# Kernel tuning notes

Measured on AMD Instinct MI355X. Metric: run time of the kernel, lower is better.

Reference implementation:

```python
import jax, jax.numpy as jnp
from jax import lax
import numpy as np

LSTM = 128      # encoder hidden per direction
H2 = 2 * LSTM   # decoder hidden / bi-encoder output dim
E = 1024        # embedding dim
V = 30611       # vocab
A = 64          # attention dim
B, S, T = 16, 400, 96
START_TOK = 101


def setup_inputs() -> dict:
    key = jax.random.key(0)
    ks = jax.random.split(key, 24)
    d = {}
    d["word_embedding"] = jax.random.normal(ks[0], (V, E), jnp.float32) * 0.05
    d["article"] = jax.random.randint(ks[1], (B, S), 0, V)
    d["article_length"] = jax.random.randint(ks[2], (B,), S // 2, S + 1)
    d["abstract"] = jax.random.randint(ks[3], (B, T), 0, V)

    def p(k, shape, scale):
        return jax.random.normal(k, shape, jnp.float32) * scale

    # encoder BiLSTM (PyTorch gate order i,f,g,o), forward and backward dirs
    d["enc_Wih_f"] = p(ks[4], (4 * LSTM, E), 0.03)
    d["enc_Whh_f"] = p(ks[5], (4 * LSTM, LSTM), 0.08)
    d["enc_b_f"] = jnp.zeros((4 * LSTM,), jnp.float32)
    d["enc_Wih_b"] = p(ks[6], (4 * LSTM, E), 0.03)
    d["enc_Whh_b"] = p(ks[7], (4 * LSTM, LSTM), 0.08)
    d["enc_b_b"] = jnp.zeros((4 * LSTM,), jnp.float32)
    # decoder LSTM: input = embed(1024) + context(256)
    d["dec_Wih"] = p(ks[8], (4 * H2, E + H2), 0.03)
    d["dec_Whh"] = p(ks[9], (4 * H2, H2), 0.06)
    d["dec_b"] = jnp.zeros((4 * H2,), jnp.float32)
    # vocab prediction
    d["pred_W"] = p(ks[10], (V, H2), 0.06)
    d["pred_b"] = jnp.zeros((V,), jnp.float32)
    # additive attention
    d["attn_s_W"] = p(ks[11], (A, H2), 0.06)
    d["attn_s_b"] = jnp.zeros((A,), jnp.float32)
    d["attn_h_W"] = p(ks[12], (A, H2), 0.06)
    d["attn_h_b"] = jnp.zeros((A,), jnp.float32)
    d["attn_f_W"] = p(ks[13], (1, A), 0.12)
    d["attn_f_b"] = jnp.zeros((1,), jnp.float32)
    return d


def _lstm_cell(x, h, c, Wih, Whh, b):
    g = x @ Wih.T + h @ Whh.T + b
    i, f, gg, o = jnp.split(g, 4, axis=-1)
    c = jax.nn.sigmoid(f) * c + jax.nn.sigmoid(i) * jnp.tanh(gg)
    h = jax.nn.sigmoid(o) * jnp.tanh(c)
    return h, c


def reference(word_embedding, article, article_length, abstract,
              enc_Wih_f, enc_Whh_f, enc_b_f, enc_Wih_b, enc_Whh_b, enc_b_b,
              dec_Wih, dec_Whh, dec_b, pred_W, pred_b,
              attn_s_W, attn_s_b, attn_h_W, attn_h_b, attn_f_W, attn_f_b):
    dt = word_embedding.dtype
    # ---- encoder ----
    xe = word_embedding[article]          # [B,S,E]
    xs = xe.transpose(1, 0, 2)            # [S,B,E]
    z = jnp.zeros((B, LSTM), dt)

    def fstep(carry, x):
        h, c = carry
        h, c = _lstm_cell(x, h, c, enc_Wih_f, enc_Whh_f, enc_b_f)
        return (h, c), h

    def bstep(carry, x):
        h, c = carry
        h, c = _lstm_cell(x, h, c, enc_Wih_b, enc_Whh_b, enc_b_b)
        return (h, c), h

    (hf, cf_f), out_f = lax.scan(fstep, (z, z), xs)
    (hb, cf_b), out_b = lax.scan(bstep, (z, z), xs, reverse=True)
    enc_out = jnp.concatenate([out_f, out_b], axis=-1).transpose(1, 0, 2)  # [B,S,2H]

    # decoder init state = concat of final fwd/bwd encoder states
    h0 = jnp.concatenate([hf, hb], axis=-1)   # [B,H2]
    c0 = jnp.concatenate([cf_f, cf_b], axis=-1)

    # attention mask: (+9999 valid, -9999 pad); min(score, mask) keeps valid scores
    length = jnp.clip(article_length, 1, S)
    pos = jnp.arange(S)
    mask = jnp.where(pos[None, :] < length[:, None], 9999.0, -9999.0).astype(dt)

    enc_ws = enc_out @ attn_s_W.T + attn_s_b  # [B,S,A], precomputed per original code

    # teacher forcing inputs: step 0 uses token 101, step t uses abstract[:, t-1]
    tokens_in = jnp.concatenate(
        [jnp.full((B, 1), START_TOK, dtype=abstract.dtype), abstract[:, :-1]], axis=1)
    emb_in = word_embedding[tokens_in].transpose(1, 0, 2)  # [T,B,E]

    def dstep(carry, emb):
        h, c, ctx = carry
        x = jnp.concatenate([emb, ctx], axis=-1)           # [B,E+H2]
        h, c = _lstm_cell(x, h, c, dec_Wih, dec_Whh, dec_b)
        logits = h @ pred_W.T + pred_b                     # [B,V]
        wh = h @ attn_h_W.T + attn_h_b                     # [B,A]
        score = jnp.tanh(enc_ws + wh[:, None, :]) @ attn_f_W[0] + attn_f_b[0]  # [B,S]
        score = jnp.minimum(score, mask)
        w = jax.nn.softmax(score, axis=-1)
        ctx = jnp.einsum('bs,bsd->bd', w, enc_out)         # [B,H2]
        return (h, c, ctx), logits

    ctx0 = jnp.zeros((B, H2), dt)
    _, logits = lax.scan(dstep, (h0, c0, ctx0), emb_in)    # [T,B,V]

    logits = logits.transpose(1, 0, 2).reshape(B * T, V)
    tgt = abstract.reshape(-1)
    logp = jax.nn.log_softmax(logits, axis=-1)
    nll = -jnp.take_along_axis(logp, tgt[:, None], axis=1)[:, 0]
    valid = (tgt != 0).astype(logits.dtype)                # ignore_index=0
    loss = jnp.sum(nll * valid) / jnp.maximum(jnp.sum(valid), 1.0)
    return loss
```

## Files before the change

kernel.cpp:

```cpp
#include <hip/hip_runtime.h>
#include <cmath>

#define NB 16
#define SS 400
#define TT 96
#define HL 128
#define HH 256
#define AA 64
#define VV 30611
#define VVP 30720
#define START_TOK 101
#define NCHUNK 120

typedef __attribute__((ext_vector_type(8))) short bf16x8;
typedef __attribute__((ext_vector_type(4))) float f32x4;

#define PIN4(v) asm volatile("" : "+v"((v).x), "+v"((v).y), "+v"((v).z), "+v"((v).w))
#define LBAR() asm volatile("s_waitcnt lgkmcnt(0)\n\ts_barrier" ::: "memory")

__device__ __forceinline__ float gload(const float* p) {
  return __hip_atomic_load(p, __ATOMIC_RELAXED, __HIP_MEMORY_SCOPE_AGENT);
}
__device__ __forceinline__ void gstore(float* p, float v) {
  __hip_atomic_store(p, v, __ATOMIC_RELAXED, __HIP_MEMORY_SCOPE_AGENT);
}
__device__ __forceinline__ float sigmf(float x) { return 1.0f / (1.0f + __expf(-x)); }
__device__ __forceinline__ float tanhf_(float x) {
  float xc = fminf(fmaxf(x, -15.0f), 15.0f);
  return 1.0f - 2.0f / (__expf(2.0f * xc) + 1.0f);
}
__device__ __forceinline__ short f2bf(float f) {
  unsigned u = __float_as_uint(f);
  unsigned r = (u + 0x7FFFu + ((u >> 16) & 1u)) >> 16;
  return (short)r;
}
__device__ __forceinline__ void flagbar(int* flags, int b, int g, int target) {
  __syncthreads();
  if (threadIdx.x == 0)
    __hip_atomic_store(&flags[b*8 + g], target, __ATOMIC_RELAXED, __HIP_MEMORY_SCOPE_AGENT);
  if (threadIdx.x < 8) {
    while (__hip_atomic_load(&flags[b*8 + threadIdx.x], __ATOMIC_RELAXED, __HIP_MEMORY_SCOPE_AGENT) < target)
      __builtin_amdgcn_s_sleep(1);
  }
  LBAR();
}

__global__ __launch_bounds__(256) void k_init(int* flags) {
  if (threadIdx.x < 128) flags[threadIdx.x] = 0;
}

__global__ __launch_bounds__(256) void k_casts(
    const float* __restrict__ wf, const float* __restrict__ wb,
    const float* __restrict__ dwih,
    short* __restrict__ wfB, short* __restrict__ wbB, short* __restrict__ dwB)
{
  const int stride = gridDim.x * 256;
  const int t0 = blockIdx.x * 256 + threadIdx.x;
  for (int i = t0; i < 512*1024; i += stride) wfB[i] = f2bf(wf[i]);
  for (int i = t0; i < 512*1024; i += stride) wbB[i] = f2bf(wb[i]);
  for (int i = t0; i < 1024*1024; i += stride) {
    int r = i >> 10, k = i & 1023;
    dwB[i] = f2bf(dwih[r*1280 + k]);
  }
}

__global__ __launch_bounds__(256) void k_embproj_enc_mfma(
    const float* __restrict__ emb, const int* __restrict__ article,
    const short* __restrict__ wfB, const short* __restrict__ wbB,
    const float* __restrict__ bf, const float* __restrict__ bb,
    float* __restrict__ xcomb)
{
  const int m0 = blockIdx.x * 64;
  const int n0 = blockIdx.y * 256;
  const int t = threadIdx.x;
  const int w = t >> 6, l = t & 63;
  __shared__ short Abuf[64*136];
  __shared__ int tok[64];
  if (t < 64) {
    int R = m0 + t, s = R >> 4, b = R & 15;
    tok[t] = article[b*SS + s];
  }
  const short* __restrict__ Wb = (n0 < 512) ? wfB : wbB;
  const int nb0 = (n0 < 512) ? n0 : (n0 - 512);
  f32x4 acc[4][4];
  #pragma unroll
  for (int i = 0; i < 4; ++i)
    #pragma unroll
    for (int j = 0; j < 4; ++j) acc[i][j] = (f32x4){0.f,0.f,0.f,0.f};
  __syncthreads();
  const int ar = t >> 2, ak0 = (t & 3) * 32;
  for (int kc = 0; kc < 8; ++kc) {
    const float* src = emb + (size_t)tok[ar]*1024 + kc*128 + ak0;
    #pragma unroll
    for (int j = 0; j < 8; ++j) {
      float4 v = *(const float4*)(src + 4*j);
      short4 s4; s4.x = f2bf(v.x); s4.y = f2bf(v.y); s4.z = f2bf(v.z); s4.w = f2bf(v.w);
      *(short4*)(&Abuf[ar*136 + ak0 + 4*j]) = s4;
    }
    LBAR();
    #pragma unroll
    for (int ks = 0; ks < 4; ++ks) {
      bf16x8 af[4];
      #pragma unroll
      for (int mr = 0; mr < 4; ++mr)
        af[mr] = *(const bf16x8*)(&Abuf[(mr*16 + (l & 15))*136 + ks*32 + (l >> 4)*8]);
      #pragma unroll
      for (int ct = 0; ct < 4; ++ct) {
        int n = nb0 + w*64 + ct*16 + (l & 15);
        bf16x8 bfr = *(const bf16x8*)(Wb + (size_t)n*1024 + kc*128 + ks*32 + (l >> 4)*8);
        #pragma unroll
        for (int mr = 0; mr < 4; ++mr)
          acc[mr][ct] = __builtin_amdgcn_mfma_f32_16x16x32_bf16(af[mr], bfr, acc[mr][ct], 0, 0, 0);
      }
    }
    LBAR();
  }
  #pragma unroll
  for (int ct = 0; ct < 4; ++ct) {
    int n = n0 + w*64 + ct*16 + (l & 15);
    float bias = (n < 512) ? bf[n] : bb[n - 512];
    #pragma unroll
    for (int mr = 0; mr < 4; ++mr) {
      #pragma unroll
      for (int r = 0; r < 4; ++r) {
        int R = m0 + mr*16 + (l >> 4)*4 + r;
        xcomb[(size_t)R*1024 + n] = acc[mr][ct][r] + bias;
      }
    }
  }
}

__global__ __launch_bounds__(256) void k_embproj_dec_mfma(
    const float* __restrict__ emb, const int* __restrict__ abstr,
    const short* __restrict__ dwB, const float* __restrict__ db,
    float* __restrict__ decpre)
{
  const int m0 = blockIdx.x * 64;
  const int n0 = blockIdx.y * 256;
  const int t = threadIdx.x;
  const int w = t >> 6, l = t & 63;
  __shared__ short Abuf[64*136];
  __shared__ int tok[64];
  if (t < 64) {
    int R = m0 + t, tt = R >> 4, b = R & 15;
    tok[t] = (tt == 0) ? START_TOK : abstr[b*TT + tt - 1];
  }
  f32x4 acc[4][4];
  #pragma unroll
  for (int i = 0; i < 4; ++i)
    #pragma unroll
    for (int j = 0; j < 4; ++j) acc[i][j] = (f32x4){0.f,0.f,0.f,0.f};
  __syncthreads();
  const int ar = t >> 2, ak0 = (t & 3) * 32;
  for (int kc = 0; kc < 8; ++kc) {
    const float* src = emb + (size_t)tok[ar]*1024 + kc*128 + ak0;
    #pragma unroll
    for (int j = 0; j < 8; ++j) {
      float4 v = *(const float4*)(src + 4*j);
      short4 s4; s4.x = f2bf(v.x); s4.y = f2bf(v.y); s4.z = f2bf(v.z); s4.w = f2bf(v.w);
      *(short4*)(&Abuf[ar*136 + ak0 + 4*j]) = s4;
    }
    LBAR();
    #pragma unroll
    for (int ks = 0; ks < 4; ++ks) {
      bf16x8 af[4];
      #pragma unroll
      for (int mr = 0; mr < 4; ++mr)
        af[mr] = *(const bf16x8*)(&Abuf[(mr*16 + (l & 15))*136 + ks*32 + (l >> 4)*8]);
      #pragma unroll
      for (int ct = 0; ct < 4; ++ct) {
        int n = n0 + w*64 + ct*16 + (l & 15);
        bf16x8 bfr = *(const bf16x8*)(dwB + (size_t)n*1024 + kc*128 + ks*32 + (l >> 4)*8);
        #pragma unroll
        for (int mr = 0; mr < 4; ++mr)
          acc[mr][ct] = __builtin_amdgcn_mfma_f32_16x16x32_bf16(af[mr], bfr, acc[mr][ct], 0, 0, 0);
      }
    }
    LBAR();
  }
  #pragma unroll
  for (int ct = 0; ct < 4; ++ct) {
    int n = n0 + w*64 + ct*16 + (l & 15);
    float bias = db[n];
    #pragma unroll
    for (int mr = 0; mr < 4; ++mr) {
      #pragma unroll
      for (int r = 0; r < 4; ++r) {
        int R = m0 + mr*16 + (l >> 4)*4 + r;
        decpre[(size_t)R*1024 + n] = acc[mr][ct][r] + bias;
      }
    }
  }
}

__global__ __launch_bounds__(1024, 4) void k_encoder(
    const float* __restrict__ xcomb,
    const float* __restrict__ whhf, const float* __restrict__ whhb,
    float* __restrict__ encout,
    float* __restrict__ hpub,
    float* __restrict__ c0buf,
    const float* __restrict__ predW, short* __restrict__ predWb)
{
  const int t = threadIdx.x;
  if (blockIdx.x >= 32) {
    const size_t idx0 = (size_t)(blockIdx.x - 32) * 1024 + t;
    const size_t stride = (size_t)224 * 1024;
    for (size_t i = idx0; i < (size_t)VVP*256; i += stride)
      predWb[i] = (i < (size_t)VV*256) ? f2bf(predW[i]) : (short)0;
    return;
  }
  const int b = blockIdx.x & 15, dir = blockIdx.x >> 4;
  const int row = t & 511;
  const int ks = t >> 9;
  const float* __restrict__ Whh = dir ? whhb : whhf;
  float4 wr[16];
  #pragma unroll
  for (int j = 0; j < 16; ++j) {
    wr[j] = *(const float4*)(Whh + row*128 + ks*64 + j*4);
    PIN4(wr[j]);
  }
  __shared__ float hl[128];
  __shared__ float part[2][512];
  float c_reg = 0.0f;
  if (t < 128) hl[t] = 0.0f;
  float xv0 = 0.f, xv1 = 0.f, xv2 = 0.f, xv3 = 0.f;
  if (t < 128) {
    const float* xr = xcomb + ((dir ? (SS-1) : 0)*NB + b)*1024 + dir*512 + t;
    xv0 = xr[0]; xv1 = xr[128]; xv2 = xr[256]; xv3 = xr[384];
  }
  __syncthreads();
  for (int s = 0; s < SS; ++s) {
    const int sf = dir ? (SS-1-s) : s;
    const float* hs = hl + ks*64;
    float a0 = 0.f, a1 = 0.f, a2 = 0.f, a3 = 0.f;
    #pragma unroll
    for (int j = 0; j < 16; j += 4) {
      float4 h0 = *(const float4*)(hs + j*4);
      float4 h1 = *(const float4*)(hs + j*4 + 4);
      float4 h2 = *(const float4*)(hs + j*4 + 8);
      float4 h3 = *(const float4*)(hs + j*4 + 12);
      a0 += wr[j].x*h0.x + wr[j].y*h0.y + wr[j].z*h0.z + wr[j].w*h0.w;
      a1 += wr[j+1].x*h1.x + wr[j+1].y*h1.y + wr[j+1].z*h1.z + wr[j+1].w*h1.w;
      a2 += wr[j+2].x*h2.x + wr[j+2].y*h2.y + wr[j+2].z*h2.z + wr[j+2].w*h2.w;
      a3 += wr[j+3].x*h3.x + wr[j+3].y*h3.y + wr[j+3].z*h3.z + wr[j+3].w*h3.w;
    }
    part[ks][row] = (a0 + a1) + (a2 + a3);
    float nx0 = 0.f, nx1 = 0.f, nx2 = 0.f, nx3 = 0.f;
    if (t < 128 && s + 1 < SS) {
      const int sfn = dir ? (SS-2-s) : (s+1);
      const float* xr = xcomb + (sfn*NB + b)*1024 + dir*512 + t;
      nx0 = xr[0]; nx1 = xr[128]; nx2 = xr[256]; nx3 = xr[384];
    }
    LBAR();
    if (t < 128) {
      float gi = part[0][t]       + part[1][t]       + xv0;
      float gf = part[0][128 + t] + part[1][128 + t] + xv1;
      float gg = part[0][256 + t] + part[1][256 + t] + xv2;
      float go = part[0][384 + t] + part[1][384 + t] + xv3;
      float iv = sigmf(gi), fv = sigmf(gf), gv = tanhf_(gg), ov = sigmf(go);
      c_reg = fv*c_reg + iv*gv;
      float hv = ov*tanhf_(c_reg);
      hl[t] = hv;
      encout[(b*SS + sf)*HH + dir*HL + t] = hv;
    }
    LBAR();
    xv0 = nx0; xv1 = nx1; xv2 = nx2; xv3 = nx3;
  }
  if (t < 128) {
    hpub[b*HH + dir*HL + t] = hl[t];
    c0buf[b*HH + dir*HL + t] = c_reg;
  }
}

__global__ __launch_bounds__(256) void k_encws(
    const float* __restrict__ encout,
    const float* __restrict__ asW, const float* __restrict__ asb,
    float* __restrict__ encwsR)
{
  const int rt = blockIdx.x;
  const int tid = threadIdx.x;
  __shared__ float Al[32*260];
  #pragma unroll
  for (int i = 0; i < 32; ++i) {
    int l = tid + i*256;
    int r = l >> 8, k = l & 255;
    Al[r*260 + k] = encout[(rt*32 + r)*256 + k];
  }
  __syncthreads();
  const int a = tid & 63, rg = tid >> 6;
  float acc[8];
  #pragma unroll
  for (int q = 0; q < 8; ++q) acc[q] = 0.0f;
  const float4* w4 = (const float4*)(asW + a*256);
  for (int k4 = 0; k4 < 64; ++k4) {
    float4 w = w4[k4];
    #pragma unroll
    for (int q = 0; q < 8; ++q) {
      const float4* a4 = (const float4*)(Al + (rg*8 + q)*260);
      float4 av = a4[k4];
      acc[q] += av.x*w.x + av.y*w.y + av.z*w.z + av.w*w.w;
    }
  }
  float bias = asb[a];
  #pragma unroll
  for (int q = 0; q < 8; ++q) {
    int row = rt*32 + rg*8 + q;
    encwsR[row*64 + a] = acc[q] + bias;
  }
}

__global__ __launch_bounds__(1024, 4) void k_decoder(
    const float* __restrict__ decpre,
    const float* __restrict__ dwhh,
    const float* __restrict__ dwih,
    const float* __restrict__ ahW, const float* __restrict__ ahb,
    const float* __restrict__ afW, const float* __restrict__ afb,
    const float* __restrict__ encwsR,
    const float* __restrict__ encout,
    const int* __restrict__ alen,
    const float* __restrict__ c0buf,
    float* hpub, float* cpub, float* wpub,
    float* __restrict__ dhall,
    int* flags)
{
  const int wg = blockIdx.x;
  const int g = wg >> 4, b = wg & 15;
  const int t = threadIdx.x;
  const int r = t & 127, ks = t >> 7;
  const int lane = t & 63;
  const int u = t & 31;
  const int s0 = g*50;

  const int grow = (r >> 5)*256 + g*32 + (r & 31);
  float4 wr[16];
  #pragma unroll
  for (int j = 0; j < 16; ++j) {
    int k = ks*64 + j*4;
    wr[j] = (k < 256) ? *(const float4*)(dwhh + grow*256 + k)
                      : *(const float4*)(dwih + grow*1280 + 1024 + (k - 256));
    PIN4(wr[j]);
  }

  __shared__ float encl[50*256];
  __shared__ float wsl[50*68];
  __shared__ float ahWt[32*68];
  __shared__ float hc[512];
  __shared__ float part[8][132];
  __shared__ float wh[64];
  __shared__ float fwl[64];
  __shared__ float scl[64];
  __shared__ float sh_m, sh_s;

  for (int i = t; i < 50*256; i += 1024) {
    int si = i >> 8, d = i & 255;
    encl[i] = encout[(b*SS + s0 + si)*HH + d];
  }
  for (int i = t; i < 50*64; i += 1024) {
    int si = i >> 6, a = i & 63;
    wsl[si*68 + a] = encwsR[(b*SS + s0 + si)*64 + a];
  }
  for (int i = t; i < 32*64; i += 1024) {
    int u2 = i >> 6, a = i & 63;
    ahWt[u2*68 + a] = ahW[a*HH + g*32 + u2];
  }
  if (t < 64) fwl[t] = afW[t];
  const float fb0 = afb[0];
  int len = alen[b]; len = min(max(len, 1), SS);
  float c_reg = 0.f;
  float pre0 = 0.f, pre1 = 0.f, pre2 = 0.f, pre3 = 0.f;
  if (t < 256) {
    c_reg = c0buf[b*HH + g*32 + u];
    hc[t] = gload(hpub + b*HH + t);
    hc[256 + t] = 0.0f;
    const float* pr = decpre + (size_t)(0*NB + b)*1024 + g*32 + u;
    pre0 = pr[0]; pre1 = pr[256]; pre2 = pr[512]; pre3 = pr[768];
  }
  __syncthreads();

  for (int tt = 0; tt < TT; ++tt) {
    {
      const float* hs = hc + ks*64;
      float a0 = 0.f, a1 = 0.f, a2 = 0.f, a3 = 0.f;
      #pragma unroll
      for (int j = 0; j < 16; j += 4) {
        float4 h0 = *(const float4*)(hs + j*4);
        float4 h1 = *(const float4*)(hs + j*4 + 4);
        float4 h2 = *(const float4*)(hs + j*4 + 8);
        float4 h3 = *(const float4*)(hs + j*4 + 12);
        a0 += wr[j].x*h0.x + wr[j].y*h0.y + wr[j].z*h0.z + wr[j].w*h0.w;
        a1 += wr[j+1].x*h1.x + wr[j+1].y*h1.y + wr[j+1].z*h1.z + wr[j+1].w*h1.w;
        a2 += wr[j+2].x*h2.x + wr[j+2].y*h2.y + wr[j+2].z*h2.z + wr[j+2].w*h2.w;
        a3 += wr[j+3].x*h3.x + wr[j+3].y*h3.y + wr[j+3].z*h3.z + wr[j+3].w*h3.w;
      }
      part[ks][r] = (a0 + a1) + (a2 + a3);
    }
    LBAR();
    if (t < 256) {
      float g0 = pre0, g1 = pre1, g2 = pre2, g3 = pre3;
      #pragma unroll
      for (int j = 0; j < 8; ++j) {
        g0 += part[j][u];
        g1 += part[j][32 + u];
        g2 += part[j][64 + u];
        g3 += part[j][96 + u];
      }
      float iv = sigmf(g0), fv = sigmf(g1), gv = tanhf_(g2), ov = sigmf(g3);
      c_reg = fv*c_reg + iv*gv;
      float hv = ov*tanhf_(c_reg);
      if (t < 32) {
        gstore(hpub + b*HH + g*32 + t, hv);
        dhall[(tt*NB + b)*HH + g*32 + t] = hv;
      }
      int wv = t >> 6;
      int a = wv*16 + (lane >> 2);
      int j4 = lane & 3;
      float wacc = 0.f;
      #pragma unroll
      for (int i = 0; i < 8; ++i) {
        int u2 = j4*8 + i;
        float hx = __shfl(hv, u2, 64);
        wacc += ahWt[u2*68 + a] * hx;
      }
      wacc += __shfl_xor(wacc, 1);
      wacc += __shfl_xor(wacc, 2);
      if (j4 == 0) gstore(wpub + (b*8 + g)*72 + a, wacc);
    }
    flagbar(flags, b, g, 2*tt + 1);
    if (t < 256) {
      hc[t] = gload(hpub + b*HH + t);
      if (tt + 1 < TT) {
        const float* pr = decpre + (size_t)((tt+1)*NB + b)*1024 + g*32 + u;
        pre0 = pr[0]; pre1 = pr[256]; pre2 = pr[512]; pre3 = pr[768];
      }
    } else if (t < 320) {
      int a = t - 256;
      float s = ahb[a];
      #pragma unroll
      for (int j = 0; j < 8; ++j) s += gload(wpub + (b*8 + j)*72 + a);
      wh[a] = s;
    }
    LBAR();
    if (t < 800) {
      int s = t >> 4, j = t & 15;
      const float* wrow = wsl + s*68 + j*4;
      float p = fwl[j*4]   * tanhf_(wrow[0] + wh[j*4])
              + fwl[j*4+1] * tanhf_(wrow[1] + wh[j*4+1])
              + fwl[j*4+2] * tanhf_(wrow[2] + wh[j*4+2])
              + fwl[j*4+3] * tanhf_(wrow[3] + wh[j*4+3]);
      p += __shfl_xor(p, 1);
      p += __shfl_xor(p, 2);
      p += __shfl_xor(p, 4);
      p += __shfl_xor(p, 8);
      if (j == 0) scl[s] = p;
    }
    LBAR();
    if (t < 64) {
      float sc = -1e30f;
      if (t < 50) {
        sc = fb0 + scl[t];
        sc = fminf(sc, (s0 + t < len) ? 9999.0f : -9999.0f);
      }
      float m = sc;
      #pragma unroll
      for (int o = 32; o; o >>= 1) m = fmaxf(m, __shfl_xor(m, o));
      float p = (t < 50) ? __expf(sc - m) : 0.0f;
      scl[t] = p;
      float ssum = p;
      #pragma unroll
      for (int o = 32; o; o >>= 1) ssum += __shfl_xor(ssum, o);
      if (t == 0) { sh_m = m; sh_s = ssum; }
    }
    LBAR();
    if (t < 256) {
      float acc = 0.0f;
      const float* eb = encl + t;
      #pragma unroll 10
      for (int i = 0; i < 50; ++i) acc += scl[i] * eb[i*256];
      gstore(cpub + (b*8 + g)*272 + t, acc);
      if (t == 0) gstore(cpub + (b*8 + g)*272 + 256, sh_m);
      if (t == 1) gstore(cpub + (b*8 + g)*272 + 257, sh_s);
    }
    flagbar(flags, b, g, 2*tt + 2);
    if (t < 256) {
      float mj[8], sj[8];
      #pragma unroll
      for (int j = 0; j < 8; ++j) {
        mj[j] = gload(cpub + (b*8 + j)*272 + 256);
        sj[j] = gload(cpub + (b*8 + j)*272 + 257);
      }
      float M = mj[0];
      #pragma unroll
      for (int j = 1; j < 8; ++j) M = fmaxf(M, mj[j]);
      float denom = 0.f, ctx = 0.f;
      #pragma unroll
      for (int j = 0; j < 8; ++j) {
        float e = __expf(mj[j] - M);
        denom += sj[j] * e;
        ctx += gload(cpub + (b*8 + j)*272 + t) * e;
      }
      hc[256 + t] = ctx / denom;
    }
    LBAR();
  }
}

__global__ __launch_bounds__(256) void k_pred_mfma(
    const float* __restrict__ dhall,
    const short* __restrict__ predWb,
    const float* __restrict__ predb,
    float* __restrict__ pm, float* __restrict__ ps)
{
  const int m0 = blockIdx.x * 64;
  const int ch = blockIdx.y;
  const int c0 = ch * 256;
  const int t = threadIdx.x;
  const int w = t >> 6, l = t & 63;
  __shared__ __align__(16) char smem[64*264*4];
  short* Abuf = (short*)smem;
  float* L    = (float*)smem;
  __shared__ float red[256];
  __shared__ float rowmax[64];

  {
    const int ar = t >> 2, ak0 = (t & 3) * 64;
    const float* src = dhall + (size_t)(m0 + ar)*256 + ak0;
    #pragma unroll
    for (int j = 0; j < 16; ++j) {
      float4 v = *(const float4*)(src + 4*j);
      short4 s4; s4.x = f2bf(v.x); s4.y = f2bf(v.y); s4.z = f2bf(v.z); s4.w = f2bf(v.w);
      *(short4*)(&Abuf[ar*264 + ak0 + 4*j]) = s4;
    }
  }
  LBAR();
  f32x4 acc[4][4];
  #pragma unroll
  for (int i = 0; i < 4; ++i)
    #pragma unroll
    for (int j = 0; j < 4; ++j) acc[i][j] = (f32x4){0.f,0.f,0.f,0.f};
  #pragma unroll
  for (int kst = 0; kst < 8; ++kst) {
    bf16x8 af[4];
    #pragma unroll
    for (int mr = 0; mr < 4; ++mr)
      af[mr] = *(const bf16x8*)(&Abuf[(mr*16 + (l & 15))*264 + kst*32 + (l >> 4)*8]);
    #pragma unroll
    for (int ct = 0; ct < 4; ++ct) {
      int col = c0 + w*64 + ct*16 + (l & 15);
      bf16x8 bfr = *(const bf16x8*)(predWb + (size_t)col*256 + kst*32 + (l >> 4)*8);
      #pragma unroll
      for (int mr = 0; mr < 4; ++mr)
        acc[mr][ct] = __builtin_amdgcn_mfma_f32_16x16x32_bf16(af[mr], bfr, acc[mr][ct], 0, 0, 0);
    }
  }
  LBAR();
  #pragma unroll
  for (int ct = 0; ct < 4; ++ct) {
    int col = c0 + w*64 + ct*16 + (l & 15);
    float bias = (col < VV) ? predb[col] : 0.0f;
    bool valid = (col < VV);
    #pragma unroll
    for (int mr = 0; mr < 4; ++mr) {
      #pragma unroll
      for (int r = 0; r < 4; ++r) {
        int rl = mr*16 + (l >> 4)*4 + r;
        L[rl*264 + w*64 + ct*16 + (l & 15)] = valid ? (acc[mr][ct][r] + bias) : -1e30f;
      }
    }
  }
  LBAR();
  {
    const int row = t & 63, qd = t >> 6;
    float m = -1e30f;
    const float* Lr = L + row*264 + qd*64;
    for (int i = 0; i < 64; ++i) m = fmaxf(m, Lr[i]);
    red[qd*64 + row] = m;
  }
  LBAR();
  if (t < 64) {
    float m = fmaxf(fmaxf(red[t], red[64+t]), fmaxf(red[128+t], red[192+t]));
    rowmax[t] = m;
  }
  LBAR();
  {
    const int row = t & 63, qd = t >> 6;
    float m = rowmax[row];
    float ssum = 0.f;
    const float* Lr = L + row*264 + qd*64;
    for (int i = 0; i < 64; ++i) ssum += __expf(Lr[i] - m);
    red[qd*64 + row] = ssum;
  }
  LBAR();
  if (t < 64) {
    float ssum = red[t] + red[64+t] + red[128+t] + red[192+t];
    pm[(m0 + t)*NCHUNK + ch] = rowmax[t];
    ps[(m0 + t)*NCHUNK + ch] = ssum;
  }
}

__global__ __launch_bounds__(256) void k_loss_part(
    const float* __restrict__ pm, const float* __restrict__ ps,
    const float* __restrict__ dhall,
    const float* __restrict__ predW, const float* __restrict__ predb,
    const int* __restrict__ abstr, float* __restrict__ lpart)
{
  const int tid = threadIdx.x;
  const int row = blockIdx.x*256 + tid;
  __shared__ float rs[256], rc[256];
  float lsum = 0.0f, lcnt = 0.0f;
  {
    int t = row >> 4, b = row & 15;
    int tok = abstr[b*TT + t];
    float m = -1e30f;
    for (int c = 0; c < NCHUNK; ++c) m = fmaxf(m, pm[row*NCHUNK + c]);
    float ss = 0.0f;
    for (int c = 0; c < NCHUNK; ++c) ss += ps[row*NCHUNK + c] * __expf(pm[row*NCHUNK + c] - m);
    float lse = m + __logf(ss);
    float tl = predb[tok];
    const float* hrow = dhall + row*256;
    const float* wrow = predW + tok*256;
    #pragma unroll 4
    for (int k = 0; k < 256; ++k) tl += hrow[k] * wrow[k];
    if (tok != 0) { lsum = lse - tl; lcnt = 1.0f; }
  }
  rs[tid] = lsum; rc[tid] = lcnt;
  __syncthreads();
  for (int st = 128; st; st >>= 1) {
    if (tid < st) { rs[tid] += rs[tid + st]; rc[tid] += rc[tid + st]; }
    __syncthreads();
  }
  if (tid == 0) { lpart[blockIdx.x*2] = rs[0]; lpart[blockIdx.x*2 + 1] = rc[0]; }
}

__global__ void k_loss_final(const float* __restrict__ lpart, float* __restrict__ out) {
  if (threadIdx.x == 0) {
    float s = 0.f, c = 0.f;
    for (int i = 0; i < 6; ++i) { s += lpart[i*2]; c += lpart[i*2 + 1]; }
    out[0] = s / fmaxf(c, 1.0f);
  }
}

extern "C" void kernel_launch(void* const* d_in, const int* in_sizes, int n_in,
                              void* d_out, int out_size, void* d_ws, size_t ws_size,
                              hipStream_t stream) {
  const float* emb   = (const float*)d_in[0];
  const int* article = (const int*)d_in[1];
  const int* alen    = (const int*)d_in[2];
  const int* abstr   = (const int*)d_in[3];
  const float* eWihF = (const float*)d_in[4];
  const float* eWhhF = (const float*)d_in[5];
  const float* ebF   = (const float*)d_in[6];
  const float* eWihB = (const float*)d_in[7];
  const float* eWhhB = (const float*)d_in[8];
  const float* ebB   = (const float*)d_in[9];
  const float* dWih  = (const float*)d_in[10];
  const float* dWhh  = (const float*)d_in[11];
  const float* db    = (const float*)d_in[12];
  const float* pW    = (const float*)d_in[13];
  const float* pb    = (const float*)d_in[14];
  const float* asW   = (const float*)d_in[15];
  const float* asb   = (const float*)d_in[16];
  const float* ahW   = (const float*)d_in[17];
  const float* ahb   = (const float*)d_in[18];
  const float* afW   = (const float*)d_in[19];
  const float* afb   = (const float*)d_in[20];
  float* out = (float*)d_out;

  float* w = (float*)d_ws;
  size_t o = 0;
  float* xcomb  = w + o; o += (size_t)SS*NB*1024;
  float* encout = w + o; o += (size_t)NB*SS*HH;
  float* encwsR = w + o; o += (size_t)NB*SS*AA;
  float* decpre = w + o; o += (size_t)TT*NB*1024;
  float* dhall  = w + o; o += (size_t)TT*NB*HH;
  float* hpub   = w + o; o += NB*HH;
  float* cpub   = w + o; o += NB*8*272;
  float* wpub   = w + o; o += NB*8*72;
  float* c0buf  = w + o; o += NB*HH;
  float* pm     = w + o; o += (size_t)TT*NB*NCHUNK;
  float* ps     = w + o; o += (size_t)TT*NB*NCHUNK;
  float* lpart  = w + o; o += 16;
  int* flags = (int*)(w + o); o += 128;
  short* predWb = (short*)(w + o); o += (size_t)VVP*256/2;
  short* wfB    = (short*)(w + o); o += 512*1024/2;
  short* wbB    = (short*)(w + o); o += 512*1024/2;
  short* dwB    = (short*)(w + o); o += 1024*1024/2;

  k_init<<<1, 256, 0, stream>>>(flags);
  k_casts<<<512, 256, 0, stream>>>(eWihF, eWihB, dWih, wfB, wbB, dwB);
  k_embproj_enc_mfma<<<dim3(100, 4), 256, 0, stream>>>(emb, article, wfB, wbB, ebF, ebB, xcomb);
  k_embproj_dec_mfma<<<dim3(24, 4), 256, 0, stream>>>(emb, abstr, dwB, db, decpre);
  k_encoder<<<256, 1024, 0, stream>>>(xcomb, eWhhF, eWhhB, encout, hpub, c0buf, pW, predWb);
  k_encws<<<200, 256, 0, stream>>>(encout, asW, asb, encwsR);
  k_decoder<<<128, 1024, 0, stream>>>(decpre, dWhh, dWih, ahW, ahb, afW, afb,
                                      encwsR, encout, alen, c0buf, hpub, cpub, wpub, dhall, flags);
  k_pred_mfma<<<dim3(24, 120), 256, 0, stream>>>(dhall, predWb, pb, pm, ps);
  k_loss_part<<<6, 256, 0, stream>>>(pm, ps, dhall, pW, pb, abstr, lpart);
  k_loss_final<<<1, 64, 0, stream>>>(lpart, out);
}
```

Baseline: 1.624 ms.

## Precompute encoder outputs projected through decoder context weights, drop second grid barrier

Since the decoder's context input feeds into its input weights linearly, the context-part weights are applied ahead of time to every encoder output. A new MFMA branch in the encws kernel produces a bf16 per-position projection, stored in the reused xcomb buffer. Each decoder workgroup then computes attention over all 400 positions locally and accumulates its own gate contributions from that projection. This removes the cross-workgroup context exchange and one flag barrier per step, and halves the per-thread recurrent weights. The costs are redundant attention scoring in all 8 workgroups per batch, more bf16 reads each step, and a change in rounding.

```diff
diff --git a/kernel.cpp b/kernel.cpp
--- a/kernel.cpp
+++ b/kernel.cpp
@@ -34,6 +34,9 @@
   unsigned r = (u + 0x7FFFu + ((u >> 16) & 1u)) >> 16;
   return (short)r;
 }
+__device__ __forceinline__ float bf2f(unsigned short s) {
+  return __uint_as_float(((unsigned)s) << 16);
+}
 __device__ __forceinline__ void flagbar(int* flags, int b, int g, int target) {
   __syncthreads();
   if (threadIdx.x == 0)
@@ -52,7 +55,8 @@
 __global__ __launch_bounds__(256) void k_casts(
     const float* __restrict__ wf, const float* __restrict__ wb,
     const float* __restrict__ dwih,
-    short* __restrict__ wfB, short* __restrict__ wbB, short* __restrict__ dwB)
+    short* __restrict__ wfB, short* __restrict__ wbB, short* __restrict__ dwB,
+    short* __restrict__ dwCb)
 {
   const int stride = gridDim.x * 256;
   const int t0 = blockIdx.x * 256 + threadIdx.x;
@@ -61,6 +65,10 @@
   for (int i = t0; i < 1024*1024; i += stride) {
     int r = i >> 10, k = i & 1023;
     dwB[i] = f2bf(dwih[r*1280 + k]);
+  }
+  for (int i = t0; i < 1024*256; i += stride) {
+    int n = i >> 8, k = i & 255;
+    dwCb[i] = f2bf(dwih[n*1280 + 1024 + k]);
   }
 }
 
@@ -272,54 +280,107 @@
   }
 }
 
-__global__ __launch_bounds__(256) void k_encws(
+__global__ __launch_bounds__(256) void k_encws_proj(
     const float* __restrict__ encout,
     const float* __restrict__ asW, const float* __restrict__ asb,
-    float* __restrict__ encwsR)
+    float* __restrict__ encwsR,
+    const short* __restrict__ dwCb,
+    short* __restrict__ encprojB)
 {
-  const int rt = blockIdx.x;
   const int tid = threadIdx.x;
-  __shared__ float Al[32*260];
-  #pragma unroll
-  for (int i = 0; i < 32; ++i) {
-    int l = tid + i*256;
-    int r = l >> 8, k = l & 255;
-    Al[r*260 + k] = encout[(rt*32 + r)*256 + k];
-  }
-  __syncthreads();
-  const int a = tid & 63, rg = tid >> 6;
-  float acc[8];
-  #pragma unroll
-  for (int q = 0; q < 8; ++q) acc[q] = 0.0f;
-  const float4* w4 = (const float4*)(asW + a*256);
-  for (int k4 = 0; k4 < 64; ++k4) {
-    float4 w = w4[k4];
+  if (blockIdx.x < 200) {
+    const int rt = blockIdx.x;
+    __shared__ float Al[32*260];
+    #pragma unroll
+    for (int i = 0; i < 32; ++i) {
+      int l = tid + i*256;
+      int r = l >> 8, k = l & 255;
+      Al[r*260 + k] = encout[(rt*32 + r)*256 + k];
+    }
+    __syncthreads();
+    const int a = tid & 63, rg = tid >> 6;
+    float acc[8];
+    #pragma unroll
+    for (int q = 0; q < 8; ++q) acc[q] = 0.0f;
+    const float4* w4 = (const float4*)(asW + a*256);
+    for (int k4 = 0; k4 < 64; ++k4) {
+      float4 w = w4[k4];
+      #pragma unroll
+      for (int q = 0; q < 8; ++q) {
+        const float4* a4 = (const float4*)(Al + (rg*8 + q)*260);
+        float4 av = a4[k4];
+        acc[q] += av.x*w.x + av.y*w.y + av.z*w.z + av.w*w.w;
+      }
+    }
+    float bias = asb[a];
     #pragma unroll
     for (int q = 0; q < 8; ++q) {
-      const float4* a4 = (const float4*)(Al + (rg*8 + q)*260);
-      float4 av = a4[k4];
-      acc[q] += av.x*w.x + av.y*w.y + av.z*w.z + av.w*w.w;
-    }
-  }
-  float bias = asb[a];
-  #pragma unroll
-  for (int q = 0; q < 8; ++q) {
-    int row = rt*32 + rg*8 + q;
-    encwsR[row*64 + a] = acc[q] + bias;
+      int row = rt*32 + rg*8 + q;
+      encwsR[row*64 + a] = acc[q] + bias;
+    }
+  } else {
+    const int bid = blockIdx.x - 200;
+    const int m0 = (bid >> 2) * 64;
+    const int c0 = (bid & 3) * 256;
+    const int t = tid;
+    const int w = t >> 6, l = t & 63;
+    __shared__ short Abuf[64*264];
+    {
+      const int ar = t >> 2, ak0 = (t & 3) * 64;
+      const float* src = encout + (size_t)(m0 + ar)*256 + ak0;
+      #pragma unroll
+      for (int j = 0; j < 16; ++j) {
+        float4 v = *(const float4*)(src + 4*j);
+        short4 s4; s4.x = f2bf(v.x); s4.y = f2bf(v.y); s4.z = f2bf(v.z); s4.w = f2bf(v.w);
+        *(short4*)(&Abuf[ar*264 + ak0 + 4*j]) = s4;
+      }
+    }
+    LBAR();
+    f32x4 acc[4][4];
+    #pragma unroll
+    for (int i = 0; i < 4; ++i)
+      #pragma unroll
+      for (int j = 0; j < 4; ++j) acc[i][j] = (f32x4){0.f,0.f,0.f,0.f};
+    #pragma unroll
+    for (int kst = 0; kst < 8; ++kst) {
+      bf16x8 af[4];
+      #pragma unroll
+      for (int mr = 0; mr < 4; ++mr)
+        af[mr] = *(const bf16x8*)(&Abuf[(mr*16 + (l & 15))*264 + kst*32 + (l >> 4)*8]);
+      #pragma unroll
+      for (int ct = 0; ct < 4; ++ct) {
+        int col = c0 + w*64 + ct*16 + (l & 15);
+        bf16x8 bfr = *(const bf16x8*)(dwCb + (size_t)col*256 + kst*32 + (l >> 4)*8);
+        #pragma unroll
+        for (int mr = 0; mr < 4; ++mr)
+          acc[mr][ct] = __builtin_amdgcn_mfma_f32_16x16x32_bf16(af[mr], bfr, acc[mr][ct], 0, 0, 0);
+      }
+    }
+    #pragma unroll
+    for (int ct = 0; ct < 4; ++ct) {
+      int col = c0 + w*64 + ct*16 + (l & 15);
+      #pragma unroll
+      for (int mr = 0; mr < 4; ++mr) {
+        #pragma unroll
+        for (int r = 0; r < 4; ++r) {
+          int R = m0 + mr*16 + (l >> 4)*4 + r;
+          encprojB[(size_t)R*1024 + col] = f2bf(acc[mr][ct][r]);
+        }
+      }
+    }
   }
 }
 
 __global__ __launch_bounds__(1024, 4) void k_decoder(
     const float* __restrict__ decpre,
     const float* __restrict__ dwhh,
-    const float* __restrict__ dwih,
     const float* __restrict__ ahW, const float* __restrict__ ahb,
     const float* __restrict__ afW, const float* __restrict__ afb,
     const float* __restrict__ encwsR,
-    const float* __restrict__ encout,
+    const short* __restrict__ encprojB,
     const int* __restrict__ alen,
     const float* __restrict__ c0buf,
-    float* hpub, float* cpub, float* wpub,
+    float* hpub, float* wpub,
     float* __restrict__ dhall,
     int* flags)
 {
@@ -329,40 +390,34 @@
   const int r = t & 127, ks = t >> 7;
   const int lane = t & 63;
   const int u = t & 31;
-  const int s0 = g*50;
-
   const int grow = (r >> 5)*256 + g*32 + (r & 31);
-  float4 wr[16];
-  #pragma unroll
-  for (int j = 0; j < 16; ++j) {
-    int k = ks*64 + j*4;
-    wr[j] = (k < 256) ? *(const float4*)(dwhh + grow*256 + k)
-                      : *(const float4*)(dwih + grow*1280 + 1024 + (k - 256));
+
+  float4 wr[8];
+  #pragma unroll
+  for (int j = 0; j < 8; ++j) {
+    wr[j] = *(const float4*)(dwhh + grow*256 + ks*32 + j*4);
     PIN4(wr[j]);
   }
 
-  __shared__ float encl[50*256];
-  __shared__ float wsl[50*68];
+  __shared__ float wsl[400*68 + 16];
   __shared__ float ahWt[32*68];
-  __shared__ float hc[512];
+  __shared__ float hsh[256];
   __shared__ float part[8][132];
+  __shared__ float part2[8][132];
   __shared__ float wh[64];
   __shared__ float fwl[64];
-  __shared__ float scl[64];
-  __shared__ float sh_m, sh_s;
-
-  for (int i = t; i < 50*256; i += 1024) {
-    int si = i >> 8, d = i & 255;
-    encl[i] = encout[(b*SS + s0 + si)*HH + d];
-  }
-  for (int i = t; i < 50*64; i += 1024) {
+  __shared__ float scl[448];
+  __shared__ float red[16];
+
+  for (int i = t; i < 400*64; i += 1024) {
     int si = i >> 6, a = i & 63;
-    wsl[si*68 + a] = encwsR[(b*SS + s0 + si)*64 + a];
+    wsl[si*68 + a] = encwsR[(b*SS + si)*64 + a];
   }
   for (int i = t; i < 32*64; i += 1024) {
     int u2 = i >> 6, a = i & 63;
     ahWt[u2*68 + a] = ahW[a*HH + g*32 + u2];
   }
+  for (int i = t; i < 8*132; i += 1024) ((float*)part2)[i] = 0.0f;
   if (t < 64) fwl[t] = afW[t];
   const float fb0 = afb[0];
   int len = alen[b]; len = min(max(len, 1), SS);
@@ -370,8 +425,7 @@
   float pre0 = 0.f, pre1 = 0.f, pre2 = 0.f, pre3 = 0.f;
   if (t < 256) {
     c_reg = c0buf[b*HH + g*32 + u];
-    hc[t] = gload(hpub + b*HH + t);
-    hc[256 + t] = 0.0f;
+    hsh[t] = gload(hpub + b*HH + t);
     const float* pr = decpre + (size_t)(0*NB + b)*1024 + g*32 + u;
     pre0 = pr[0]; pre1 = pr[256]; pre2 = pr[512]; pre3 = pr[768];
   }
@@ -379,30 +433,26 @@
 
   for (int tt = 0; tt < TT; ++tt) {
     {
-      const float* hs = hc + ks*64;
-      float a0 = 0.f, a1 = 0.f, a2 = 0.f, a3 = 0.f;
-      #pragma unroll
-      for (int j = 0; j < 16; j += 4) {
+      const float* hs = hsh + ks*32;
+      float a0 = 0.f, a1 = 0.f;
+      #pragma unroll
+      for (int j = 0; j < 8; j += 2) {
         float4 h0 = *(const float4*)(hs + j*4);
         float4 h1 = *(const float4*)(hs + j*4 + 4);
-        float4 h2 = *(const float4*)(hs + j*4 + 8);
-        float4 h3 = *(const float4*)(hs + j*4 + 12);
         a0 += wr[j].x*h0.x + wr[j].y*h0.y + wr[j].z*h0.z + wr[j].w*h0.w;
         a1 += wr[j+1].x*h1.x + wr[j+1].y*h1.y + wr[j+1].z*h1.z + wr[j+1].w*h1.w;
-        a2 += wr[j+2].x*h2.x + wr[j+2].y*h2.y + wr[j+2].z*h2.z + wr[j+2].w*h2.w;
-        a3 += wr[j+3].x*h3.x + wr[j+3].y*h3.y + wr[j+3].z*h3.z + wr[j+3].w*h3.w;
-      }
-      part[ks][r] = (a0 + a1) + (a2 + a3);
+      }
+      part[ks][r] = a0 + a1;
     }
     LBAR();
     if (t < 256) {
       float g0 = pre0, g1 = pre1, g2 = pre2, g3 = pre3;
       #pragma unroll
       for (int j = 0; j < 8; ++j) {
-        g0 += part[j][u];
-        g1 += part[j][32 + u];
-        g2 += part[j][64 + u];
-        g3 += part[j][96 + u];
+        g0 += part[j][u]      + part2[j][u];
+        g1 += part[j][32 + u] + part2[j][32 + u];
+        g2 += part[j][64 + u] + part2[j][64 + u];
+        g3 += part[j][96 + u] + part2[j][96 + u];
       }
       float iv = sigmf(g0), fv = sigmf(g1), gv = tanhf_(g2), ov = sigmf(g3);
       c_reg = fv*c_reg + iv*gv;
@@ -425,13 +475,12 @@
       wacc += __shfl_xor(wacc, 2);
       if (j4 == 0) gstore(wpub + (b*8 + g)*72 + a, wacc);
     }
-    flagbar(flags, b, g, 2*tt + 1);
+    flagbar(flags, b, g, tt + 1);
+    if (tt == TT - 1) break;
     if (t < 256) {
-      hc[t] = gload(hpub + b*HH + t);
-      if (tt + 1 < TT) {
-        const float* pr = decpre + (size_t)((tt+1)*NB + b)*1024 + g*32 + u;
-        pre0 = pr[0]; pre1 = pr[256]; pre2 = pr[512]; pre3 = pr[768];
-      }
+      hsh[t] = gload(hpub + b*HH + t);
+      const float* pr = decpre + (size_t)((tt+1)*NB + b)*1024 + g*32 + u;
+      pre0 = pr[0]; pre1 = pr[256]; pre2 = pr[512]; pre3 = pr[768];
     } else if (t < 320) {
       int a = t - 256;
       float s = ahb[a];
@@ -441,64 +490,53 @@
     }
     LBAR();
     if (t < 800) {
-      int s = t >> 4, j = t & 15;
-      const float* wrow = wsl + s*68 + j*4;
-      float p = fwl[j*4]   * tanhf_(wrow[0] + wh[j*4])
-              + fwl[j*4+1] * tanhf_(wrow[1] + wh[j*4+1])
-              + fwl[j*4+2] * tanhf_(wrow[2] + wh[j*4+2])
-              + fwl[j*4+3] * tanhf_(wrow[3] + wh[j*4+3]);
+      int s = t >> 1, half = t & 1;
+      const float* wrow = wsl + s*68 + half*32;
+      const float* whh = wh + half*32;
+      const float* fw = fwl + half*32;
+      float p = 0.f;
+      #pragma unroll
+      for (int j = 0; j < 32; ++j) p += fw[j] * tanhf_(wrow[j] + whh[j]);
       p += __shfl_xor(p, 1);
-      p += __shfl_xor(p, 2);
-      p += __shfl_xor(p, 4);
-      p += __shfl_xor(p, 8);
-      if (j == 0) scl[s] = p;
-    }
-    LBAR();
-    if (t < 64) {
-      float sc = -1e30f;
-      if (t < 50) {
-        sc = fb0 + scl[t];
-        sc = fminf(sc, (s0 + t < len) ? 9999.0f : -9999.0f);
-      }
-      float m = sc;
+      if (half == 0) {
+        float sc = fb0 + p;
+        sc = fminf(sc, (s < len) ? 9999.0f : -9999.0f);
+        scl[s] = sc;
+      }
+    }
+    LBAR();
+    {
+      float v = (t < 400) ? scl[t] : -1e30f;
+      float m = v;
       #pragma unroll
       for (int o = 32; o; o >>= 1) m = fmaxf(m, __shfl_xor(m, o));
-      float p = (t < 50) ? __expf(sc - m) : 0.0f;
-      scl[t] = p;
+      if (t < 448 && lane == 0) red[t >> 6] = m;
+    }
+    LBAR();
+    {
+      float M = red[0];
+      #pragma unroll
+      for (int i = 1; i < 7; ++i) M = fmaxf(M, red[i]);
+      float p = (t < 400) ? __expf(scl[t] - M) : 0.0f;
+      if (t < 400) scl[t] = p;
       float ssum = p;
       #pragma unroll
       for (int o = 32; o; o >>= 1) ssum += __shfl_xor(ssum, o);
-      if (t == 0) { sh_m = m; sh_s = ssum; }
-    }
-    LBAR();
-    if (t < 256) {
-      float acc = 0.0f;
-      const float* eb = encl + t;
+      if (t < 448 && lane == 0) red[8 + (t >> 6)] = ssum;
+    }
+    LBAR();
+    {
+      float ssum = red[8];
+      #pragma unroll
+      for (int i = 9; i < 15; ++i) ssum += red[i];
+      float inv = 1.0f / ssum;
+      const unsigned short* ep = (const unsigned short*)(encprojB) +
+                                 (size_t)(b*SS + ks*50)*1024 + grow;
+      float acc = 0.f;
       #pragma unroll 10
-      for (int i = 0; i < 50; ++i) acc += scl[i] * eb[i*256];
-      gstore(cpub + (b*8 + g)*272 + t, acc);
-      if (t == 0) gstore(cpub + (b*8 + g)*272 + 256, sh_m);
-      if (t == 1) gstore(cpub + (b*8 + g)*272 + 257, sh_s);
-    }
-    flagbar(flags, b, g, 2*tt + 2);
-    if (t < 256) {
-      float mj[8], sj[8];
-      #pragma unroll
-      for (int j = 0; j < 8; ++j) {
-        mj[j] = gload(cpub + (b*8 + j)*272 + 256);
-        sj[j] = gload(cpub + (b*8 + j)*272 + 257);
-      }
-      float M = mj[0];
-      #pragma unroll
-      for (int j = 1; j < 8; ++j) M = fmaxf(M, mj[j]);
-      float denom = 0.f, ctx = 0.f;
-      #pragma unroll
-      for (int j = 0; j < 8; ++j) {
-        float e = __expf(mj[j] - M);
-        denom += sj[j] * e;
-        ctx += gload(cpub + (b*8 + j)*272 + t) * e;
-      }
-      hc[256 + t] = ctx / denom;
+      for (int i = 0; i < 50; ++i)
+        acc += scl[ks*50 + i] * bf2f(ep[(size_t)i*1024]);
+      part2[ks][r] = acc * inv;
     }
     LBAR();
   }
@@ -673,7 +711,6 @@
   float* decpre = w + o; o += (size_t)TT*NB*1024;
   float* dhall  = w + o; o += (size_t)TT*NB*HH;
   float* hpub   = w + o; o += NB*HH;
-  float* cpub   = w + o; o += NB*8*272;
   float* wpub   = w + o; o += NB*8*72;
   float* c0buf  = w + o; o += NB*HH;
   float* pm     = w + o; o += (size_t)TT*NB*NCHUNK;
@@ -684,15 +721,17 @@
   short* wfB    = (short*)(w + o); o += 512*1024/2;
   short* wbB    = (short*)(w + o); o += 512*1024/2;
   short* dwB    = (short*)(w + o); o += 1024*1024/2;
+  short* dwCb   = (short*)(w + o); o += 1024*256/2;
+  short* encprojB = (short*)xcomb;
 
   k_init<<<1, 256, 0, stream>>>(flags);
-  k_casts<<<512, 256, 0, stream>>>(eWihF, eWihB, dWih, wfB, wbB, dwB);
+  k_casts<<<512, 256, 0, stream>>>(eWihF, eWihB, dWih, wfB, wbB, dwB, dwCb);
   k_embproj_enc_mfma<<<dim3(100, 4), 256, 0, stream>>>(emb, article, wfB, wbB, ebF, ebB, xcomb);
   k_embproj_dec_mfma<<<dim3(24, 4), 256, 0, stream>>>(emb, abstr, dwB, db, decpre);
   k_encoder<<<256, 1024, 0, stream>>>(xcomb, eWhhF, eWhhB, encout, hpub, c0buf, pW, predWb);
-  k_encws<<<200, 256, 0, stream>>>(encout, asW, asb, encwsR);
-  k_decoder<<<128, 1024, 0, stream>>>(decpre, dWhh, dWih, ahW, ahb, afW, afb,
-                                      encwsR, encout, alen, c0buf, hpub, cpub, wpub, dhall, flags);
+  k_encws_proj<<<600, 256, 0, stream>>>(encout, asW, asb, encwsR, dwCb, encprojB);
+  k_decoder<<<128, 1024, 0, stream>>>(decpre, dWhh, ahW, ahb, afW, afb,
+                                      encwsR, encprojB, alen, c0buf, hpub, wpub, dhall, flags);
   k_pred_mfma<<<dim3(24, 120), 256, 0, stream>>>(dhall, predWb, pb, pm, ps);
   k_loss_part<<<6, 256, 0, stream>>>(pm, ps, dhall, pW, pb, abstr, lpart);
   k_loss_final<<<1, 64, 0, stream>>>(lpart, out);
```

After: 1.655 ms. Within noise of the previous version (+1.9%).
